# Optimization experiments

Measured on AMD Instinct MI355X. Metric: run time of the kernel, lower is better.

## Reference

```python
import jax, jax.numpy as jnp
import numpy as np

EMBED_DIM = 1024
NUM_HEADS = 16
HEAD_DIM = EMBED_DIM // NUM_HEADS
B, S = 4, 2048


def setup_inputs() -> dict:
    key = jax.random.key(0)
    ks = jax.random.split(key, 9)
    scale = 1.0 / np.sqrt(EMBED_DIM)
    x = jax.random.normal(ks[0], (B, S, EMBED_DIM), dtype=jnp.float32)
    Wq = jax.random.uniform(ks[1], (EMBED_DIM, EMBED_DIM), jnp.float32, -scale, scale)
    bq = jax.random.uniform(ks[2], (EMBED_DIM,), jnp.float32, -scale, scale)
    Wk = jax.random.uniform(ks[3], (EMBED_DIM, EMBED_DIM), jnp.float32, -scale, scale)
    bk = jax.random.uniform(ks[4], (EMBED_DIM,), jnp.float32, -scale, scale)
    Wv = jax.random.uniform(ks[5], (EMBED_DIM, EMBED_DIM), jnp.float32, -scale, scale)
    bv = jax.random.uniform(ks[6], (EMBED_DIM,), jnp.float32, -scale, scale)
    Wo = jax.random.uniform(ks[7], (EMBED_DIM, EMBED_DIM), jnp.float32, -scale, scale)
    bo = jax.random.uniform(ks[8], (EMBED_DIM,), jnp.float32, -scale, scale)
    return {"x": x, "Wq": Wq, "bq": bq, "Wk": Wk, "bk": bk, "Wv": Wv, "bv": bv, "Wo": Wo, "bo": bo}


def reference(x, Wq, bq, Wk, bk, Wv, bv, Wo, bo):
    b, s, d = x.shape
    h, hd = NUM_HEADS, HEAD_DIM
    # projections -> [b, h, s, hd]
    def proj(W, bias):
        return (x @ W + bias).reshape(b, s, h, hd).transpose(0, 2, 1, 3)
    q = proj(Wq, bq)
    k = proj(Wk, bk)
    v = proj(Wv, bv)
    logits = jnp.einsum('bhqd,bhkd->bhqk', q, k) / np.sqrt(hd).astype(np.float32)
    attn = jax.nn.softmax(logits, axis=-1)  # dropout p=0.0 -> identity
    vals = jnp.einsum('bhqk,bhkd->bhqd', attn, v)
    vals = vals.transpose(0, 2, 1, 3).reshape(b, s, d)
    return vals @ Wo + bo
```

## Files before the change

kernel.cpp:

```cpp
#include <hip/hip_runtime.h>

typedef unsigned short u16;
typedef unsigned int u32;
typedef __bf16 bf16x8 __attribute__((ext_vector_type(8)));
typedef float f32x4 __attribute__((ext_vector_type(4)));
typedef float f32x16 __attribute__((ext_vector_type(16)));
typedef u32 u32x4 __attribute__((ext_vector_type(4)));
typedef u32 u32x2 __attribute__((ext_vector_type(2)));

#define NBATCH 4
#define NS 2048
#define ND 1024
#define NH 16
#define HDIM 64
#define KSCALE (0.125f * 1.44269504f)

#define MFMA(a, b, c) __builtin_amdgcn_mfma_f32_16x16x32_bf16(a, b, c, 0, 0, 0)
#define MFMA32(a, b, c) __builtin_amdgcn_mfma_f32_32x32x16_bf16(a, b, c, 0, 0, 0)

__device__ __forceinline__ u16 f2bf(float f) {
    u32 u = __builtin_bit_cast(u32, f);
    u += 0x7fffu + ((u >> 16) & 1u);
    return (u16)(u >> 16);
}

__device__ __forceinline__ u32 cvtpk(float a, float b) {
    u32 r;
    asm("v_cvt_pk_bf16_f32 %0, %1, %2" : "=v"(r) : "v"(a), "v"(b));
    return r;
}

__device__ __forceinline__ bf16x8 ldfrag(const u16* p) {
    u32x4 v = *(const u32x4*)p;
    return __builtin_bit_cast(bf16x8, v);
}

__device__ __forceinline__ void gld16(u16* lds, const u16* g) {
    __builtin_amdgcn_global_load_lds((__attribute__((address_space(1))) u32*)g,
                                     (__attribute__((address_space(3))) u32*)lds, 16, 0, 0);
}


__global__ __launch_bounds__(256) void cvt_tile(const float* __restrict__ src, u16* __restrict__ dst) {
    const int tile = blockIdx.x;
    const int mt = tile >> 5, ktile = tile & 31;
    const int tid = threadIdx.x;
    u16* out = dst + (size_t)tile * 4096;
#pragma unroll
    for (int half = 0; half < 2; ++half) {
        const int s = half * 256 + tid;
        const int rg = s >> 6, l = s & 63;
        const int row = mt * 128 + rg * 16 + (l & 15);
        const int col = ktile * 32 + (l >> 4) * 8;
        const float* sp = src + (size_t)row * ND + col;
        float4 v0 = *(const float4*)sp;
        float4 v1 = *(const float4*)(sp + 4);
        u32x4 o;
        o[0] = (u32)f2bf(v0.x) | ((u32)f2bf(v0.y) << 16);
        o[1] = (u32)f2bf(v0.z) | ((u32)f2bf(v0.w) << 16);
        o[2] = (u32)f2bf(v1.x) | ((u32)f2bf(v1.y) << 16);
        o[3] = (u32)f2bf(v1.z) | ((u32)f2bf(v1.w) << 16);
        *(u32x4*)(out + s * 8) = o;
    }
}

__global__ __launch_bounds__(256) void wtrans4(const float* __restrict__ W0, const float* __restrict__ W1,
                                               const float* __restrict__ W2, const float* __restrict__ W3,
                                               u16* __restrict__ T0, u16* __restrict__ T1,
                                               u16* __restrict__ T2, u16* __restrict__ T3) {
    const int z = blockIdx.z;
    const float* W = z == 0 ? W0 : z == 1 ? W1 : z == 2 ? W2 : W3;
    u16* WT = z == 0 ? T0 : z == 1 ? T1 : z == 2 ? T2 : T3;
    __shared__ u16 t[64][72];
    const int tid = threadIdx.x;
    const int k0 = blockIdx.x * 64, n0 = blockIdx.y * 64;
    {
        const int r = tid >> 2, cq = (tid & 3) * 16;
#pragma unroll
        for (int i = 0; i < 4; ++i) {
            float4 v = *(const float4*)(W + (size_t)(k0 + r) * ND + n0 + cq + i * 4);
            t[r][cq + i * 4 + 0] = f2bf(v.x);
            t[r][cq + i * 4 + 1] = f2bf(v.y);
            t[r][cq + i * 4 + 2] = f2bf(v.z);
            t[r][cq + i * 4 + 3] = f2bf(v.w);
        }
    }
    __syncthreads();
    {
        const int rr = tid >> 2, cq = (tid & 3) * 16;
        u32x4 o0, o1;
#pragma unroll
        for (int j = 0; j < 4; ++j) {
            o0[j] = (u32)t[cq + 2 * j][rr] | ((u32)t[cq + 2 * j + 1][rr] << 16);
            o1[j] = (u32)t[cq + 8 + 2 * j][rr] | ((u32)t[cq + 8 + 2 * j + 1][rr] << 16);
        }
        const int n_g = n0 + rr;
        const int nt = n_g >> 7, rgn = (n_g >> 4) & 7, lr = n_g & 15;
        const int k_g = k0 + cq;
        const int kt2 = k_g >> 5, lg = (k_g >> 3) & 3;
        u16* outb = WT + ((size_t)(nt * 32 + kt2)) * 4096 + rgn * 512 + lr * 8;
        *(u32x4*)(outb + lg * 128) = o0;
        *(u32x4*)(outb + (lg + 1) * 128) = o1;
    }
}

template <bool PF>
__device__ __forceinline__ void gemm_step(const bf16x8 (&a)[4], const bf16x8 (&b)[4],
                                          bf16x8 (&an)[4], bf16x8 (&bn)[4],
                                          const u16* aw, const u16* bw, int kt,
                                          f32x4 (&acc)[4][4]) {
    if (PF) {
        const u16* ap = aw + (size_t)(kt + 1) * 4096;
        const u16* bp = bw + (size_t)(kt + 1) * 4096;
#pragma unroll
        for (int i = 0; i < 4; ++i) {
            an[i] = ldfrag(ap + i * 512);
            bn[i] = ldfrag(bp + i * 512);
        }
    }
    __builtin_amdgcn_s_setprio(1);
#pragma unroll
    for (int mb = 0; mb < 4; ++mb)
#pragma unroll
        for (int nb = 0; nb < 4; ++nb)
            acc[mb][nb] = MFMA(a[mb], b[nb], acc[mb][nb]);
    __builtin_amdgcn_s_setprio(0);
}

__global__ __launch_bounds__(256, 3) void gemm_qkv(const u16* __restrict__ A,
                                                   const u16* __restrict__ wqT, const u16* __restrict__ wkT,
                                                   const u16* __restrict__ wvT,
                                                   const float* __restrict__ bq, const float* __restrict__ bk,
                                                   const float* __restrict__ bv,
                                                   u16* __restrict__ Qp, u16* __restrict__ Kf,
                                                   u16* __restrict__ Vf) {
    const int wg = blockIdx.x;
    const int xcd = wg & 7, idx = wg >> 3;
    const int ybl = xcd * 8 + idx / 24;
    const int xbl = idx % 24;
    const int region = xbl >> 3;
    const int m0 = ybl * 128, n0 = (xbl & 7) * 128;
    const u16* Bt = region == 0 ? wqT : region == 1 ? wkT : wvT;
    const float* bias = region == 0 ? bq : region == 1 ? bk : bv;

    const int tid = threadIdx.x;
    const int l = tid & 63, w = tid >> 6;
    const int lr = l & 15, lg = l >> 4;
    const int wr = w >> 1, wc = w & 1;

    const u16* aw = A + (size_t)ybl * 32 * 4096 + wr * 2048 + l * 8;
    const u16* bw = Bt + (size_t)(xbl & 7) * 32 * 4096 + wc * 2048 + l * 8;

    f32x4 acc[4][4] = {};
    bf16x8 aA[4], bA[4], aB[4], bB[4];
#pragma unroll
    for (int i = 0; i < 4; ++i) {
        aA[i] = ldfrag(aw + i * 512);
        bA[i] = ldfrag(bw + i * 512);
    }

    for (int kt = 0; kt < 32; kt += 2) {
        gemm_step<true>(aA, bA, aB, bB, aw, bw, kt, acc);
        if (kt + 2 < 32)
            gemm_step<true>(aB, bB, aA, bA, aw, bw, kt + 1, acc);
        else
            gemm_step<false>(aB, bB, aA, bA, aw, bw, kt + 1, acc);
    }

#pragma unroll
    for (int mb = 0; mb < 4; ++mb) {
#pragma unroll
        for (int nb = 0; nb < 4; ++nb) {
            const int col = n0 + wc * 64 + nb * 16 + lr;
            const float bia = bias[col];
            const int hd = col & 63, h = col >> 6;
            if (region == 2) {
                const int rowb = m0 + wr * 64 + mb * 16 + lg * 4;
                const int b = rowb >> 11, kv = rowb & 2047;
                const int bh = b * NH + h;
                const int ktp = kv >> 6, ks = (kv >> 4) & 3, hif = (kv >> 3) & 1, j0 = kv & 7;
                const int lane = (hd & 31) | (hif << 5);
                u32x2 o;
                o[0] = (u32)f2bf(acc[mb][nb][0] + bia) | ((u32)f2bf(acc[mb][nb][1] + bia) << 16);
                o[1] = (u32)f2bf(acc[mb][nb][2] + bia) | ((u32)f2bf(acc[mb][nb][3] + bia) << 16);
                size_t off = (size_t)bh * 131072 + (size_t)ktp * 4096 +
                             (size_t)(((ks + 4 * (hd >> 5)) * 64 + lane) * 8 + j0);
                *(u32x2*)(Vf + off) = o;
            } else if (region == 1) {
#pragma unroll
                for (int r = 0; r < 4; ++r) {
                    const int rowg = m0 + wr * 64 + mb * 16 + lg * 4 + r;
                    float v = (acc[mb][nb][r] + bia) * KSCALE;
                    const int b = rowg >> 11, kv = rowg & 2047;
                    const int bh = b * NH + h;
                    const int ktp = kv >> 6, kvb = (kv >> 5) & 1;
                    const int lane = (kv & 31) | (((hd >> 3) & 1) << 5);
                    size_t o = (size_t)bh * 131072 + (size_t)ktp * 4096 +
                               (size_t)(((kvb * 4 + (hd >> 4)) * 64 + lane) * 8 + (hd & 7));
                    Kf[o] = f2bf(v);
                }
            } else {
#pragma unroll
                for (int r = 0; r < 4; ++r) {
                    const int rowg = m0 + wr * 64 + mb * 16 + lg * 4 + r;
                    float v = acc[mb][nb][r] + bia;
                    size_t o = ((size_t)((rowg >> 11) * NH + h) * NS + (rowg & 2047)) * HDIM + hd;
                    Qp[o] = f2bf(v);
                }
            }
        }
    }
}

__global__ __launch_bounds__(256, 3) void gemm_o(const u16* __restrict__ A, const u16* __restrict__ Bt,
                                                 const float* __restrict__ bias, float* __restrict__ of32) {
    const int wg = blockIdx.x;
    const int xcd = wg & 7, idx = wg >> 3;
    const int ybl = xcd * 8 + (idx >> 3);
    const int xbl = idx & 7;
    const int m0 = ybl * 128, n0 = xbl * 128;

    const int tid = threadIdx.x;
    const int l = tid & 63, w = tid >> 6;
    const int lr = l & 15, lg = l >> 4;
    const int wr = w >> 1, wc = w & 1;

    const u16* aw = A + (size_t)ybl * 32 * 4096 + wr * 2048 + l * 8;
    const u16* bw = Bt + (size_t)xbl * 32 * 4096 + wc * 2048 + l * 8;

    f32x4 acc[4][4] = {};
    bf16x8 aA[4], bA[4], aB[4], bB[4];
#pragma unroll
    for (int i = 0; i < 4; ++i) {
        aA[i] = ldfrag(aw + i * 512);
        bA[i] = ldfrag(bw + i * 512);
    }

    for (int kt = 0; kt < 32; kt += 2) {
        gemm_step<true>(aA, bA, aB, bB, aw, bw, kt, acc);
        if (kt + 2 < 32)
            gemm_step<true>(aB, bB, aA, bA, aw, bw, kt + 1, acc);
        else
            gemm_step<false>(aB, bB, aA, bA, aw, bw, kt + 1, acc);
    }

#pragma unroll
    for (int mb = 0; mb < 4; ++mb) {
#pragma unroll
        for (int nb = 0; nb < 4; ++nb) {
            const int col = n0 + wc * 64 + nb * 16 + lr;
            const float bia = bias[col];
#pragma unroll
            for (int r = 0; r < 4; ++r) {
                const int rowg = m0 + wr * 64 + mb * 16 + lg * 4 + r;
                of32[(size_t)rowg * ND + col] = acc[mb][nb][r] + bia;
            }
        }
    }
}

__global__ __launch_bounds__(256, 3) void attn(const u16* __restrict__ Q, const u16* __restrict__ Kf,
                                               const u16* __restrict__ Vf, u16* __restrict__ AO) {
    __shared__ u16 sm[16384];
    const int tid = threadIdx.x;
    const int l = tid & 63, w = tid >> 6;
    const int lq = l & 31, hi = l >> 5;
    const int wg = blockIdx.x;
    const int xcd = wg & 7, idx = wg >> 3;
    const int bh = xcd * 8 + (idx >> 4);
    const int qb = idx & 15;
    const int qbase = qb * 128 + w * 32;

    const u16* Qrow = Q + ((size_t)bh * NS + qbase + lq) * HDIM;
    bf16x8 qf[4];
#pragma unroll
    for (int kh = 0; kh < 4; ++kh) qf[kh] = ldfrag(Qrow + kh * 16 + hi * 8);

    f32x16 oacc[2] = {};
    float ls0 = 0.f, ls1 = 0.f, ls2 = 0.f, ls3 = 0.f;

    const u16* KfB = Kf + (size_t)bh * 131072;
    const u16* VfB = Vf + (size_t)bh * 131072;

    gld16(sm + tid * 8, KfB + tid * 8);
    gld16(sm + (256 + tid) * 8, KfB + (256 + tid) * 8);
    gld16(sm + 8192 + tid * 8, VfB + tid * 8);
    gld16(sm + 8192 + (256 + tid) * 8, VfB + (256 + tid) * 8);
    __syncthreads();

    for (int kt = 0; kt < 32; ++kt) {
        const int cur = kt & 1;
        if (kt < 31) {
            const u16* kg = KfB + (size_t)(kt + 1) * 4096;
            const u16* vg = VfB + (size_t)(kt + 1) * 4096;
            u16* kd = sm + (cur ^ 1) * 4096;
            u16* vd = sm + 8192 + (cur ^ 1) * 4096;
            gld16(kd + tid * 8, kg + tid * 8);
            gld16(kd + (256 + tid) * 8, kg + (256 + tid) * 8);
            gld16(vd + tid * 8, vg + tid * 8);
            gld16(vd + (256 + tid) * 8, vg + (256 + tid) * 8);
        }
        const u16* klb = sm + cur * 4096;
        const u16* vlb = sm + 8192 + cur * 4096;

        bf16x8 kf[2][4];
#pragma unroll
        for (int kvb = 0; kvb < 2; ++kvb)
#pragma unroll
            for (int kh = 0; kh < 4; ++kh)
                kf[kvb][kh] = ldfrag(klb + ((kvb * 4 + kh) * 64 + l) * 8);

        f32x16 sacc[2] = {};
        __builtin_amdgcn_s_setprio(1);
#pragma unroll
        for (int kvb = 0; kvb < 2; ++kvb)
#pragma unroll
            for (int kh = 0; kh < 4; ++kh)
                sacc[kvb] = MFMA32(kf[kvb][kh], qf[kh], sacc[kvb]);
        __builtin_amdgcn_s_setprio(0);

        bf16x8 vf[2][4];
#pragma unroll
        for (int hdb = 0; hdb < 2; ++hdb)
#pragma unroll
            for (int ks = 0; ks < 4; ++ks)
                vf[hdb][ks] = ldfrag(vlb + ((hdb * 4 + ks) * 64 + l) * 8);

#pragma unroll
        for (int kvb = 0; kvb < 2; ++kvb) {
#pragma unroll
            for (int i = 0; i < 16; i += 4) {
                float p0 = __builtin_amdgcn_exp2f(sacc[kvb][i + 0]);
                float p1 = __builtin_amdgcn_exp2f(sacc[kvb][i + 1]);
                float p2 = __builtin_amdgcn_exp2f(sacc[kvb][i + 2]);
                float p3 = __builtin_amdgcn_exp2f(sacc[kvb][i + 3]);
                sacc[kvb][i + 0] = p0;
                sacc[kvb][i + 1] = p1;
                sacc[kvb][i + 2] = p2;
                sacc[kvb][i + 3] = p3;
                ls0 += p0;
                ls1 += p1;
                ls2 += p2;
                ls3 += p3;
            }
        }

        bf16x8 pf[4];
#pragma unroll
        for (int ks = 0; ks < 4; ++ks) {
            const int i0 = 2 * ks, i1 = 2 * ks + 1;
            const int q20 = i0 & 3, kvb0 = i0 >> 2;
            const int q21 = i1 & 3, kvb1 = i1 >> 2;
            u32 W00 = cvtpk(sacc[kvb0][4 * q20 + 0], sacc[kvb0][4 * q20 + 1]);
            u32 W01 = cvtpk(sacc[kvb0][4 * q20 + 2], sacc[kvb0][4 * q20 + 3]);
            u32 W10 = cvtpk(sacc[kvb1][4 * q21 + 0], sacc[kvb1][4 * q21 + 1]);
            u32 W11 = cvtpk(sacc[kvb1][4 * q21 + 2], sacc[kvb1][4 * q21 + 3]);
            u32x2 s0 = __builtin_amdgcn_permlane32_swap(W00, W10, false, false);
            u32x2 s1 = __builtin_amdgcn_permlane32_swap(W01, W11, false, false);
            u32x4 words;
            words[0] = s0[0];
            words[1] = s1[0];
            words[2] = s0[1];
            words[3] = s1[1];
            pf[ks] = __builtin_bit_cast(bf16x8, words);
        }

        __builtin_amdgcn_s_setprio(1);
#pragma unroll
        for (int hdb = 0; hdb < 2; ++hdb)
#pragma unroll
            for (int ks = 0; ks < 4; ++ks)
                oacc[hdb] = MFMA32(vf[hdb][ks], pf[ks], oacc[hdb]);
        __builtin_amdgcn_s_setprio(0);

        __syncthreads();
    }

    float lsum = (ls0 + ls1) + (ls2 + ls3);
    lsum += __shfl_xor(lsum, 32);

    u16* ot = sm + w * 2048;
    const float inv = 1.f / lsum;
#pragma unroll
    for (int hdb = 0; hdb < 2; ++hdb)
#pragma unroll
        for (int q2 = 0; q2 < 4; ++q2)
#pragma unroll
            for (int rp = 0; rp < 2; ++rp) {
                u32 word = cvtpk(oacc[hdb][4 * q2 + 2 * rp] * inv, oacc[hdb][4 * q2 + 2 * rp + 1] * inv);
                const int hd0 = hdb * 32 + 8 * q2 + 4 * hi + 2 * rp;
                const int byteoff = lq * 128 + ((2 * hd0) ^ ((lq & 7) << 4));
                *(u32*)((char*)ot + byteoff) = word;
            }
    const int b = bh >> 4, h = bh & 15;
#pragma unroll
    for (int p = 0; p < 4; ++p) {
        const int pidx = p * 64 + l;
        const int row = pidx >> 3;
        const int cb = ((pidx & 7) * 16) ^ ((row & 7) << 4);
        u32x4 val = *(u32x4*)((char*)ot + row * 128 + cb);
        const int m = b * NS + qbase + row;
        const int c = h * 64 + (pidx & 7) * 8;
        const int mt = m >> 7, rg = (m >> 4) & 7, lrm = m & 15;
        const int ktile = c >> 5, lgc = (c >> 3) & 3;
        *(u32x4*)(AO + ((size_t)(mt * 32 + ktile)) * 4096 + rg * 512 + (lgc * 16 + lrm) * 8) = val;
    }
}

extern "C" void kernel_launch(void* const* d_in, const int* in_sizes, int n_in,
                              void* d_out, int out_size, void* d_ws, size_t ws_size,
                              hipStream_t stream) {
    const float* x = (const float*)d_in[0];
    const float* Wq = (const float*)d_in[1];
    const float* bq = (const float*)d_in[2];
    const float* Wk = (const float*)d_in[3];
    const float* bk = (const float*)d_in[4];
    const float* Wv = (const float*)d_in[5];
    const float* bv = (const float*)d_in[6];
    const float* Wo = (const float*)d_in[7];
    const float* bo = (const float*)d_in[8];
    float* out = (float*)d_out;

    u16* ws = (u16*)d_ws;
    u16* xb = ws;
    u16* wqT = ws + 8388608;
    u16* wkT = wqT + 1048576;
    u16* wvT = wkT + 1048576;
    u16* woT = wvT + 1048576;
    u16* Qp = woT + 1048576;
    u16* Kfp = Qp + 8388608;
    u16* Vfp = Kfp + 8388608;
    u16* AO = xb;

    cvt_tile<<<2048, 256, 0, stream>>>(x, xb);
    wtrans4<<<dim3(16, 16, 4), 256, 0, stream>>>(Wq, Wk, Wv, Wo, wqT, wkT, wvT, woT);
    gemm_qkv<<<1536, 256, 0, stream>>>(xb, wqT, wkT, wvT, bq, bk, bv, Qp, Kfp, Vfp);
    attn<<<1024, 256, 0, stream>>>(Qp, Kfp, Vfp, AO);
    gemm_o<<<512, 256, 0, stream>>>(AO, woT, bo, out);
}
```

Before: 185.6 us.

## Software-pipeline attention QK and PV stages and fuse prep kernels

Restructures the attention loop so the QK^T MFMAs for tile t overlap the exp/convert/PV work of tile t-1, using alternating score accumulators and a triple-buffered V region in LDS. This is meant to hide the softmax VALU latency behind matrix work. It also merges the input conversion and weight transpose kernels into a single launch to cut launch overhead. It costs more LDS and registers, which may pressure occupancy at three blocks per CU.

```diff
diff --git a/kernel.cpp b/kernel.cpp
--- a/kernel.cpp
+++ b/kernel.cpp
@@ -41,39 +41,40 @@
 }
 
 
-__global__ __launch_bounds__(256) void cvt_tile(const float* __restrict__ src, u16* __restrict__ dst) {
-    const int tile = blockIdx.x;
-    const int mt = tile >> 5, ktile = tile & 31;
+__global__ __launch_bounds__(256) void prep(const float* __restrict__ x, const float* __restrict__ W0,
+                                            const float* __restrict__ W1, const float* __restrict__ W2,
+                                            const float* __restrict__ W3, u16* __restrict__ xb,
+                                            u16* __restrict__ T0, u16* __restrict__ T1,
+                                            u16* __restrict__ T2, u16* __restrict__ T3) {
+    __shared__ u16 t[64][72];
+    const int wg = blockIdx.x;
     const int tid = threadIdx.x;
-    u16* out = dst + (size_t)tile * 4096;
-#pragma unroll
-    for (int half = 0; half < 2; ++half) {
-        const int s = half * 256 + tid;
-        const int rg = s >> 6, l = s & 63;
-        const int row = mt * 128 + rg * 16 + (l & 15);
-        const int col = ktile * 32 + (l >> 4) * 8;
-        const float* sp = src + (size_t)row * ND + col;
-        float4 v0 = *(const float4*)sp;
-        float4 v1 = *(const float4*)(sp + 4);
-        u32x4 o;
-        o[0] = (u32)f2bf(v0.x) | ((u32)f2bf(v0.y) << 16);
-        o[1] = (u32)f2bf(v0.z) | ((u32)f2bf(v0.w) << 16);
-        o[2] = (u32)f2bf(v1.x) | ((u32)f2bf(v1.y) << 16);
-        o[3] = (u32)f2bf(v1.z) | ((u32)f2bf(v1.w) << 16);
-        *(u32x4*)(out + s * 8) = o;
-    }
-}
-
-__global__ __launch_bounds__(256) void wtrans4(const float* __restrict__ W0, const float* __restrict__ W1,
-                                               const float* __restrict__ W2, const float* __restrict__ W3,
-                                               u16* __restrict__ T0, u16* __restrict__ T1,
-                                               u16* __restrict__ T2, u16* __restrict__ T3) {
-    const int z = blockIdx.z;
+    if (wg < 2048) {
+        const int mt = wg >> 5, ktile = wg & 31;
+        u16* out = xb + (size_t)wg * 4096;
+#pragma unroll
+        for (int half = 0; half < 2; ++half) {
+            const int s = half * 256 + tid;
+            const int rg = s >> 6, l = s & 63;
+            const int row = mt * 128 + rg * 16 + (l & 15);
+            const int col = ktile * 32 + (l >> 4) * 8;
+            const float* sp = x + (size_t)row * ND + col;
+            float4 v0 = *(const float4*)sp;
+            float4 v1 = *(const float4*)(sp + 4);
+            u32x4 o;
+            o[0] = (u32)f2bf(v0.x) | ((u32)f2bf(v0.y) << 16);
+            o[1] = (u32)f2bf(v0.z) | ((u32)f2bf(v0.w) << 16);
+            o[2] = (u32)f2bf(v1.x) | ((u32)f2bf(v1.y) << 16);
+            o[3] = (u32)f2bf(v1.z) | ((u32)f2bf(v1.w) << 16);
+            *(u32x4*)(out + s * 8) = o;
+        }
+        return;
+    }
+    const int tt = wg - 2048;
+    const int z = tt >> 8, r8 = tt & 255;
     const float* W = z == 0 ? W0 : z == 1 ? W1 : z == 2 ? W2 : W3;
     u16* WT = z == 0 ? T0 : z == 1 ? T1 : z == 2 ? T2 : T3;
-    __shared__ u16 t[64][72];
-    const int tid = threadIdx.x;
-    const int k0 = blockIdx.x * 64, n0 = blockIdx.y * 64;
+    const int k0 = (r8 & 15) * 64, n0 = (r8 >> 4) * 64;
     {
         const int r = tid >> 2, cq = (tid & 3) * 16;
 #pragma unroll
@@ -261,7 +262,7 @@
 
 __global__ __launch_bounds__(256, 3) void attn(const u16* __restrict__ Q, const u16* __restrict__ Kf,
                                                const u16* __restrict__ Vf, u16* __restrict__ AO) {
-    __shared__ u16 sm[16384];
+    __shared__ u16 sm[20480];
     const int tid = threadIdx.x;
     const int l = tid & 63, w = tid >> 6;
     const int lq = l & 31, hi = l >> 5;
@@ -277,84 +278,41 @@
     for (int kh = 0; kh < 4; ++kh) qf[kh] = ldfrag(Qrow + kh * 16 + hi * 8);
 
     f32x16 oacc[2] = {};
+    f32x16 sA[2] = {}, sB[2] = {};
     float ls0 = 0.f, ls1 = 0.f, ls2 = 0.f, ls3 = 0.f;
 
     const u16* KfB = Kf + (size_t)bh * 131072;
     const u16* VfB = Vf + (size_t)bh * 131072;
 
-    gld16(sm + tid * 8, KfB + tid * 8);
-    gld16(sm + (256 + tid) * 8, KfB + (256 + tid) * 8);
-    gld16(sm + 8192 + tid * 8, VfB + tid * 8);
-    gld16(sm + 8192 + (256 + tid) * 8, VfB + (256 + tid) * 8);
-    __syncthreads();
-
-    for (int kt = 0; kt < 32; ++kt) {
-        const int cur = kt & 1;
-        if (kt < 31) {
-            const u16* kg = KfB + (size_t)(kt + 1) * 4096;
-            const u16* vg = VfB + (size_t)(kt + 1) * 4096;
-            u16* kd = sm + (cur ^ 1) * 4096;
-            u16* vd = sm + 8192 + (cur ^ 1) * 4096;
-            gld16(kd + tid * 8, kg + tid * 8);
-            gld16(kd + (256 + tid) * 8, kg + (256 + tid) * 8);
-            gld16(vd + tid * 8, vg + tid * 8);
-            gld16(vd + (256 + tid) * 8, vg + (256 + tid) * 8);
-        }
-        const u16* klb = sm + cur * 4096;
-        const u16* vlb = sm + 8192 + cur * 4096;
-
-        bf16x8 kf[2][4];
-#pragma unroll
-        for (int kvb = 0; kvb < 2; ++kvb)
-#pragma unroll
-            for (int kh = 0; kh < 4; ++kh)
-                kf[kvb][kh] = ldfrag(klb + ((kvb * 4 + kh) * 64 + l) * 8);
-
-        f32x16 sacc[2] = {};
-        __builtin_amdgcn_s_setprio(1);
-#pragma unroll
-        for (int kvb = 0; kvb < 2; ++kvb)
-#pragma unroll
-            for (int kh = 0; kh < 4; ++kh)
-                sacc[kvb] = MFMA32(kf[kvb][kh], qf[kh], sacc[kvb]);
-        __builtin_amdgcn_s_setprio(0);
-
-        bf16x8 vf[2][4];
-#pragma unroll
-        for (int hdb = 0; hdb < 2; ++hdb)
-#pragma unroll
-            for (int ks = 0; ks < 4; ++ks)
-                vf[hdb][ks] = ldfrag(vlb + ((hdb * 4 + ks) * 64 + l) * 8);
-
+    auto finish = [&](f32x16(&prv)[2], const u16* vlb) {
 #pragma unroll
         for (int kvb = 0; kvb < 2; ++kvb) {
 #pragma unroll
             for (int i = 0; i < 16; i += 4) {
-                float p0 = __builtin_amdgcn_exp2f(sacc[kvb][i + 0]);
-                float p1 = __builtin_amdgcn_exp2f(sacc[kvb][i + 1]);
-                float p2 = __builtin_amdgcn_exp2f(sacc[kvb][i + 2]);
-                float p3 = __builtin_amdgcn_exp2f(sacc[kvb][i + 3]);
-                sacc[kvb][i + 0] = p0;
-                sacc[kvb][i + 1] = p1;
-                sacc[kvb][i + 2] = p2;
-                sacc[kvb][i + 3] = p3;
+                float p0 = __builtin_amdgcn_exp2f(prv[kvb][i + 0]);
+                float p1 = __builtin_amdgcn_exp2f(prv[kvb][i + 1]);
+                float p2 = __builtin_amdgcn_exp2f(prv[kvb][i + 2]);
+                float p3 = __builtin_amdgcn_exp2f(prv[kvb][i + 3]);
+                prv[kvb][i + 0] = p0;
+                prv[kvb][i + 1] = p1;
+                prv[kvb][i + 2] = p2;
+                prv[kvb][i + 3] = p3;
                 ls0 += p0;
                 ls1 += p1;
                 ls2 += p2;
                 ls3 += p3;
             }
         }
-
         bf16x8 pf[4];
 #pragma unroll
         for (int ks = 0; ks < 4; ++ks) {
             const int i0 = 2 * ks, i1 = 2 * ks + 1;
             const int q20 = i0 & 3, kvb0 = i0 >> 2;
             const int q21 = i1 & 3, kvb1 = i1 >> 2;
-            u32 W00 = cvtpk(sacc[kvb0][4 * q20 + 0], sacc[kvb0][4 * q20 + 1]);
-            u32 W01 = cvtpk(sacc[kvb0][4 * q20 + 2], sacc[kvb0][4 * q20 + 3]);
-            u32 W10 = cvtpk(sacc[kvb1][4 * q21 + 0], sacc[kvb1][4 * q21 + 1]);
-            u32 W11 = cvtpk(sacc[kvb1][4 * q21 + 2], sacc[kvb1][4 * q21 + 3]);
+            u32 W00 = cvtpk(prv[kvb0][4 * q20 + 0], prv[kvb0][4 * q20 + 1]);
+            u32 W01 = cvtpk(prv[kvb0][4 * q20 + 2], prv[kvb0][4 * q20 + 3]);
+            u32 W10 = cvtpk(prv[kvb1][4 * q21 + 0], prv[kvb1][4 * q21 + 1]);
+            u32 W11 = cvtpk(prv[kvb1][4 * q21 + 2], prv[kvb1][4 * q21 + 3]);
             u32x2 s0 = __builtin_amdgcn_permlane32_swap(W00, W10, false, false);
             u32x2 s1 = __builtin_amdgcn_permlane32_swap(W01, W11, false, false);
             u32x4 words;
@@ -364,17 +322,60 @@
             words[3] = s1[1];
             pf[ks] = __builtin_bit_cast(bf16x8, words);
         }
-
-        __builtin_amdgcn_s_setprio(1);
-#pragma unroll
-        for (int hdb = 0; hdb < 2; ++hdb)
-#pragma unroll
-            for (int ks = 0; ks < 4; ++ks)
-                oacc[hdb] = MFMA32(vf[hdb][ks], pf[ks], oacc[hdb]);
-        __builtin_amdgcn_s_setprio(0);
-
+#pragma unroll
+        for (int hdb = 0; hdb < 2; ++hdb) {
+            bf16x8 vf[4];
+#pragma unroll
+            for (int ks = 0; ks < 4; ++ks) vf[ks] = ldfrag(vlb + ((hdb * 4 + ks) * 64 + l) * 8);
+            __builtin_amdgcn_s_setprio(1);
+#pragma unroll
+            for (int ks = 0; ks < 4; ++ks) oacc[hdb] = MFMA32(vf[ks], pf[ks], oacc[hdb]);
+            __builtin_amdgcn_s_setprio(0);
+        }
+    };
+
+    auto body = [&](int t, f32x16(&cur)[2], f32x16(&prv)[2], int dofin, int dostage) {
+        if (dostage) {
+            const u16* kg = KfB + (size_t)(t + 1) * 4096;
+            const u16* vg = VfB + (size_t)(t + 1) * 4096;
+            u16* kd = sm + ((t + 1) & 1) * 4096;
+            u16* vd = sm + 8192 + ((t + 1) % 3) * 4096;
+            gld16(kd + tid * 8, kg + tid * 8);
+            gld16(kd + (256 + tid) * 8, kg + (256 + tid) * 8);
+            gld16(vd + tid * 8, vg + tid * 8);
+            gld16(vd + (256 + tid) * 8, vg + (256 + tid) * 8);
+        }
+        const u16* klb = sm + (t & 1) * 4096;
+        f32x16 zv = {};
+        cur[0] = zv;
+        cur[1] = zv;
+#pragma unroll
+        for (int kvb = 0; kvb < 2; ++kvb) {
+            bf16x8 kf[4];
+#pragma unroll
+            for (int kh = 0; kh < 4; ++kh) kf[kh] = ldfrag(klb + ((kvb * 4 + kh) * 64 + l) * 8);
+            __builtin_amdgcn_s_setprio(1);
+#pragma unroll
+            for (int kh = 0; kh < 4; ++kh) cur[kvb] = MFMA32(kf[kh], qf[kh], cur[kvb]);
+            __builtin_amdgcn_s_setprio(0);
+        }
+        if (dofin) finish(prv, sm + 8192 + ((t - 1) % 3) * 4096);
         __syncthreads();
-    }
+    };
+
+    gld16(sm + tid * 8, KfB + tid * 8);
+    gld16(sm + (256 + tid) * 8, KfB + (256 + tid) * 8);
+    gld16(sm + 8192 + tid * 8, VfB + tid * 8);
+    gld16(sm + 8192 + (256 + tid) * 8, VfB + (256 + tid) * 8);
+    __syncthreads();
+
+    body(0, sA, sB, 0, 1);
+    for (int t = 1; t < 31; t += 2) {
+        body(t, sB, sA, 1, 1);
+        body(t + 1, sA, sB, 1, 1);
+    }
+    body(31, sB, sA, 1, 0);
+    finish(sB, sm + 8192 + (31 % 3) * 4096);
 
     float lsum = (ls0 + ls1) + (ls2 + ls3);
     lsum += __shfl_xor(lsum, 32);
@@ -432,8 +433,7 @@
     u16* Vfp = Kfp + 8388608;
     u16* AO = xb;
 
-    cvt_tile<<<2048, 256, 0, stream>>>(x, xb);
-    wtrans4<<<dim3(16, 16, 4), 256, 0, stream>>>(Wq, Wk, Wv, Wo, wqT, wkT, wvT, woT);
+    prep<<<3072, 256, 0, stream>>>(x, Wq, Wk, Wv, Wo, xb, wqT, wkT, wvT, woT);
     gemm_qkv<<<1536, 256, 0, stream>>>(xb, wqT, wkT, wvT, bq, bk, bv, Qp, Kfp, Vfp);
     attn<<<1024, 256, 0, stream>>>(Qp, Kfp, Vfp, AO);
     gemm_o<<<512, 256, 0, stream>>>(AO, woT, bo, out);
```

Result: no change. 183.5 us (-1.1%).
